# Optimization experiments

Measured on AMD Instinct MI355X. Metric: run time of the kernel, lower is better.

Reference implementation:

```python
import jax, jax.numpy as jnp
import numpy as np

WINDOW = 128  # window_length (overlap-and-add hop); K = 2*WINDOW


def setup_inputs() -> dict:
    key = jax.random.key(0)
    k_x, k_w1, k_b1, k_w2, k_b2 = jax.random.split(key, 5)
    B, D, K, S = 4, 128, 256, 256      # batch, in_channels, segment len, n segments
    C, E, O = 2, 128, 256              # source_num, encoded_frame_dim, out_channels
    x = jax.random.normal(k_x, (B, D, K, S), dtype=jnp.float32)
    prelu_w = jnp.asarray(0.25, dtype=jnp.float32)  # nn.PReLU default init
    conv1_w = jax.random.normal(k_w1, (C * E, D), dtype=jnp.float32) * 0.02
    conv1_b = jax.random.normal(k_b1, (C * E,), dtype=jnp.float32) * 0.02
    conv2_w = jax.random.normal(k_w2, (O, E), dtype=jnp.float32) * 0.02
    conv2_b = jax.random.normal(k_b2, (O,), dtype=jnp.float32) * 0.02
    return {
        "x": x,
        "prelu_w": prelu_w,
        "conv1_w": conv1_w,
        "conv1_b": conv1_b,
        "conv2_w": conv2_w,
        "conv2_b": conv2_b,
        "pad_front": 64,
        "pad_back": 64,
    }


def overlap_and_add(y, hop):
    # y: [B, C, E, S, K] -> [B, C, E, hop*(S-1)+K] windowed scatter-sum
    B, C, E, S, K = y.shape
    T = hop * (S - 1) + K
    idx = (hop * jnp.arange(S)[:, None] + jnp.arange(K)[None, :]).reshape(-1)  # [S*K]
    out = jnp.zeros((B, C, E, T), dtype=y.dtype)
    return out.at[..., idx].add(y.reshape(B, C, E, S * K))


def reference(x, prelu_w, conv1_w, conv1_b, conv2_w, conv2_b, pad_front, pad_back):
    B, D, K, S = x.shape
    E = conv2_w.shape[1]
    C = conv1_w.shape[0] // E
    # PReLU (single shared parameter)
    x = jnp.where(x >= 0, x, prelu_w * x)
    # 1x1 Conv2d: D -> C*E channels (pure GEMM over channel dim)
    x = jnp.einsum('bdks,od->boks', x, conv1_w) + conv1_b[None, :, None, None]
    # split sources/features, move K to last: [B, C, E, S, K]
    x = x.reshape(B, C, E, K, S).transpose(0, 1, 2, 4, 3)
    x = overlap_and_add(x, WINDOW)  # [B, C, E, T]
    T = x.shape[-1]
    end = T - pad_back if pad_back else T  # replicate [pad_front:-pad_back] slicing
    x = x[:, :, :, pad_front:end]          # [B, C, E, L]
    x = jax.nn.relu(x)
    # 1x1 Conv1d: E -> O
    x = jnp.einsum('bcel,oe->bcol', x, conv2_w) + conv2_b[None, None, :, None]
    return x  # [B, C, O, L]
```

## Files before the change

kernel.cpp:

```cpp
#include <hip/hip_runtime.h>
#include <hip/hip_bf16.h>
#include <stdint.h>

#define B_   4
#define D_   128
#define K_   256
#define S_   256
#define O_   256
#define E_   128
#define LOUT 32768

typedef __attribute__((ext_vector_type(8))) short short8;
typedef __attribute__((ext_vector_type(4))) float float4v;

__device__ __forceinline__ unsigned short f2bf(float f) {
  union { float f; unsigned u; } v; v.f = f;
  unsigned r = v.u + 0x7FFF + ((v.u >> 16) & 1);
  return (unsigned short)(r >> 16);
}

__device__ __forceinline__ void gl_lds16(const void* g, void* l) {
  __builtin_amdgcn_global_load_lds(
      (const __attribute__((address_space(1))) void*)g,
      (__attribute__((address_space(3))) void*)l, 16, 0, 0);
}

__global__ void pack_w_kernel(const float* __restrict__ w1, const float* __restrict__ w2,
                              unsigned short* __restrict__ w1p, unsigned short* __restrict__ w2p) {
  int i = blockIdx.x * 256 + threadIdx.x;
  w1p[i] = f2bf(w1[i]);
  w2p[i] = f2bf(w2[i]);
}

__global__ __launch_bounds__(256) void pack_x_kernel(const float* __restrict__ x,
                                                     const float* __restrict__ prelu_w,
                                                     unsigned short* __restrict__ xp) {
  __shared__ float tile[64][65];
  int k  = blockIdx.x;
  int st = blockIdx.y & 3;
  int dt = blockIdx.y >> 2;
  int b  = blockIdx.z;
  float pw = *prelu_w;
  int t = threadIdx.x;

  {
    int sl = t & 63, dl0 = t >> 6;
    const float* src = x + ((size_t)(b * D_) * K_ + k) * S_ + st * 64 + sl;
    for (int i = 0; i < 16; ++i) {
      int dl = dl0 + i * 4;
      float v = src[(size_t)(dt * 64 + dl) * (K_ * S_)];
      tile[dl][sl] = (v >= 0.f) ? v : v * pw;
    }
  }
  __syncthreads();
  {
    int dp = (t & 31) * 2, sl0 = t >> 5;
    for (int i = 0; i < 8; ++i) {
      int sl = sl0 + i * 8;
      int s = st * 64 + sl;
      int d = dt * 64 + dp;
      unsigned v0 = f2bf(tile[dp][sl]);
      unsigned v1 = f2bf(tile[dp + 1][sl]);
      *(unsigned*)(xp + (((size_t)(b * S_ + s) * K_ + k) * D_ + d)) = v0 | (v1 << 16);
    }
  }
}

__global__ __launch_bounds__(256, 2) void fused_kernel(
    const unsigned short* __restrict__ xp,
    const unsigned short* __restrict__ w1p,
    const unsigned short* __restrict__ w2p,
    const float* __restrict__ b1,
    const float* __restrict__ b2,
    float* __restrict__ out) {
  __shared__ __align__(16) unsigned char lds[65536];

  int j = blockIdx.x;
  int b = blockIdx.y;
  int t = threadIdx.x;
  int w  = t >> 6;
  int ln64 = t & 63;
  int q  = ln64 >> 4;
  int ln = ln64 & 15;

  bool va = (j < S_);
  bool vb = (j >= 1);

  {
    bool myv = (w < 2) ? va : vb;
    if (myv) {
      int s = (w < 2) ? j : (j - 1);
      for (int i = 0; i < 16; ++i) {
        int row = (w * 16 + i) * 4 + q;
        int dblk = ln ^ (row & 15);
        const unsigned short* g = xp + (((size_t)(b * S_ + s) * K_ + row) * D_ + dblk * 8);
        gl_lds16((const void*)g, (void*)(lds + (w * 16 + i) * 1024));
      }
    }
  }

  int mtg = w * 4;
  short8 a1[4][4];
  float4v b1v[4];
  for (int m = 0; m < 4; ++m) {
    int o = (mtg + m) * 16 + ln;
    for (int ks = 0; ks < 4; ++ks)
      a1[m][ks] = *(const short8*)(w1p + (size_t)o * D_ + ks * 32 + q * 8);
    b1v[m] = *(const float4v*)(b1 + (mtg + m) * 16 + q * 4);
  }
  float bmul = (va ? 1.f : 0.f) + (vb ? 1.f : 0.f);

  __syncthreads();

  int c = w >> 1;
  int ebase = (w & 1) * 64;

  for (int p = 0; p < 8; ++p) {
    float4v acca[4], accb[4];
    for (int m = 0; m < 4; ++m) { acca[m] = (float4v)0.f; accb[m] = (float4v)0.f; }
    if (va) {
      int row = p * 16 + ln;
      for (int ks = 0; ks < 4; ++ks) {
        short8 bf = *(const short8*)(lds + row * 256 + (((ks * 4 + q) ^ ln) * 16));
        for (int m = 0; m < 4; ++m)
          acca[m] = __builtin_amdgcn_mfma_f32_16x16x32_bf16(a1[m][ks], bf, acca[m], 0, 0, 0);
      }
    }
    if (vb) {
      int row = 128 + p * 16 + ln;
      for (int ks = 0; ks < 4; ++ks) {
        short8 bf = *(const short8*)(lds + row * 256 + (((ks * 4 + q) ^ ln) * 16));
        for (int m = 0; m < 4; ++m)
          accb[m] = __builtin_amdgcn_mfma_f32_16x16x32_bf16(a1[m][ks], bf, accb[m], 0, 0, 0);
      }
    }
    __syncthreads();
    int k1 = p * 16 + ln;
    for (int m = 0; m < 4; ++m) {
      float4v zf = acca[m] + accb[m] + b1v[m] * bmul;
      unsigned long long pk =
          (unsigned long long)f2bf(fmaxf(zf[0], 0.f))
        | ((unsigned long long)f2bf(fmaxf(zf[1], 0.f)) << 16)
        | ((unsigned long long)f2bf(fmaxf(zf[2], 0.f)) << 32)
        | ((unsigned long long)f2bf(fmaxf(zf[3], 0.f)) << 48);
      int e0 = ebase + m * 16 + q * 4;
      *(unsigned long long*)(lds + (c * 128 + k1) * 256 + ((e0 >> 3) ^ ln) * 16 + (e0 & 7) * 2) = pk;
    }
  }
  __syncthreads();

  short8 a2[4][4];
  float4v b2v[4];
  for (int m = 0; m < 4; ++m) {
    int o2 = (mtg + m) * 16 + ln;
    for (int ks = 0; ks < 4; ++ks)
      a2[m][ks] = *(const short8*)(w2p + (size_t)o2 * E_ + ks * 32 + q * 8);
    b2v[m] = *(const float4v*)(b2 + (mtg + m) * 16 + q * 4);
  }

  for (int cc = 0; cc < 2; ++cc) {
    for (int nt = 0; nt < 8; ++nt) {
      float4v acc[4];
      for (int m = 0; m < 4; ++m) acc[m] = (float4v)0.f;
      int k1 = nt * 16 + ln;
      for (int ks = 0; ks < 4; ++ks) {
        short8 bf = *(const short8*)(lds + (cc * 128 + k1) * 256 + (((ks * 4 + q) ^ ln) * 16));
        for (int m = 0; m < 4; ++m)
          acc[m] = __builtin_amdgcn_mfma_f32_16x16x32_bf16(a2[m][ks], bf, acc[m], 0, 0, 0);
      }
      int lpos = j * 128 + k1 - 64;
      if (lpos >= 0 && lpos < LOUT) {
        for (int m = 0; m < 4; ++m) {
          float4v ov = acc[m] + b2v[m];
          for (int r = 0; r < 4; ++r) {
            int o2 = (mtg + m) * 16 + q * 4 + r;
            out[((size_t)(b * 2 + cc) * 256 + o2) * LOUT + lpos] = ov[r];
          }
        }
      }
    }
  }
}

extern "C" void kernel_launch(void* const* d_in, const int* in_sizes, int n_in,
                              void* d_out, int out_size, void* d_ws, size_t ws_size,
                              hipStream_t stream) {
  const float* x       = (const float*)d_in[0];
  const float* prelu_w = (const float*)d_in[1];
  const float* w1      = (const float*)d_in[2];
  const float* b1      = (const float*)d_in[3];
  const float* w2      = (const float*)d_in[4];
  const float* b2      = (const float*)d_in[5];

  unsigned short* xp  = (unsigned short*)d_ws;
  unsigned short* w1p = xp + (size_t)B_ * S_ * K_ * D_;
  unsigned short* w2p = w1p + (size_t)O_ * D_;

  pack_w_kernel<<<dim3(128), 256, 0, stream>>>(w1, w2, w1p, w2p);
  pack_x_kernel<<<dim3(K_, 8, B_), 256, 0, stream>>>(x, prelu_w, xp);
  fused_kernel<<<dim3(S_ + 1, B_), 256, 0, stream>>>(xp, w1p, w2p, b1, b2,
                                                     (float*)d_out);
}
```

Measured before the change: 437.1 us.

## Vectorize pack loads/stores and swap GEMM2 operands for float4 output stores

```diff
diff --git a/kernel.cpp b/kernel.cpp
--- a/kernel.cpp
+++ b/kernel.cpp
@@ -44,24 +44,32 @@
   int t = threadIdx.x;
 
   {
-    int sl = t & 63, dl0 = t >> 6;
-    const float* src = x + ((size_t)(b * D_) * K_ + k) * S_ + st * 64 + sl;
-    for (int i = 0; i < 16; ++i) {
-      int dl = dl0 + i * 4;
-      float v = src[(size_t)(dt * 64 + dl) * (K_ * S_)];
-      tile[dl][sl] = (v >= 0.f) ? v : v * pw;
+    int s4  = (t & 15) * 4;
+    int dl0 = t >> 4;
+    const float* src = x + ((size_t)(b * D_ + dt * 64) * K_ + k) * S_ + st * 64 + s4;
+#pragma unroll
+    for (int i = 0; i < 4; ++i) {
+      int dl = dl0 + i * 16;
+      float4v v = *(const float4v*)(src + (size_t)dl * (K_ * S_));
+#pragma unroll
+      for (int r = 0; r < 4; ++r) {
+        float f = v[r];
+        tile[dl][s4 + r] = (f >= 0.f) ? f : f * pw;
+      }
     }
   }
   __syncthreads();
   {
-    int dp = (t & 31) * 2, sl0 = t >> 5;
-    for (int i = 0; i < 8; ++i) {
-      int sl = sl0 + i * 8;
+    int d8 = (t & 7) * 8;
+    int sx = t >> 3;
+#pragma unroll
+    for (int i = 0; i < 2; ++i) {
+      int sl = sx + i * 32;
+      short8 o;
+#pragma unroll
+      for (int e = 0; e < 8; ++e) o[e] = (short)f2bf(tile[d8 + e][sl]);
       int s = st * 64 + sl;
-      int d = dt * 64 + dp;
-      unsigned v0 = f2bf(tile[dp][sl]);
-      unsigned v1 = f2bf(tile[dp + 1][sl]);
-      *(unsigned*)(xp + (((size_t)(b * S_ + s) * K_ + k) * D_ + d)) = v0 | (v1 << 16);
+      *(short8*)(xp + (((size_t)(b * S_ + s) * K_ + k) * D_ + dt * 64 + d8)) = o;
     }
   }
 }
@@ -147,35 +155,40 @@
       *(unsigned long long*)(lds + (c * 128 + k1) * 256 + ((e0 >> 3) ^ ln) * 16 + (e0 & 7) * 2) = pk;
     }
   }
+
+  short8 w2f[4][4];
+  float  b2s[4];
+  for (int n = 0; n < 4; ++n) {
+    int o2 = w * 64 + n * 16 + ln;
+    for (int ks = 0; ks < 4; ++ks)
+      w2f[n][ks] = *(const short8*)(w2p + (size_t)o2 * E_ + ks * 32 + q * 8);
+    b2s[n] = b2[o2];
+  }
+
   __syncthreads();
 
-  short8 a2[4][4];
-  float4v b2v[4];
-  for (int m = 0; m < 4; ++m) {
-    int o2 = (mtg + m) * 16 + ln;
-    for (int ks = 0; ks < 4; ++ks)
-      a2[m][ks] = *(const short8*)(w2p + (size_t)o2 * E_ + ks * 32 + q * 8);
-    b2v[m] = *(const float4v*)(b2 + (mtg + m) * 16 + q * 4);
-  }
-
   for (int cc = 0; cc < 2; ++cc) {
-    for (int nt = 0; nt < 8; ++nt) {
+    for (int m = 0; m < 8; ++m) {
+      short8 zf[4];
+#pragma unroll
+      for (int ks = 0; ks < 4; ++ks)
+        zf[ks] = *(const short8*)(lds + (cc * 128 + m * 16 + ln) * 256 + (((ks * 4 + q) ^ ln) * 16));
       float4v acc[4];
-      for (int m = 0; m < 4; ++m) acc[m] = (float4v)0.f;
-      int k1 = nt * 16 + ln;
-      for (int ks = 0; ks < 4; ++ks) {
-        short8 bf = *(const short8*)(lds + (cc * 128 + k1) * 256 + (((ks * 4 + q) ^ ln) * 16));
-        for (int m = 0; m < 4; ++m)
-          acc[m] = __builtin_amdgcn_mfma_f32_16x16x32_bf16(a2[m][ks], bf, acc[m], 0, 0, 0);
-      }
-      int lpos = j * 128 + k1 - 64;
+#pragma unroll
+      for (int n = 0; n < 4; ++n) acc[n] = (float4v)0.f;
+#pragma unroll
+      for (int ks = 0; ks < 4; ++ks)
+#pragma unroll
+        for (int n = 0; n < 4; ++n)
+          acc[n] = __builtin_amdgcn_mfma_f32_16x16x32_bf16(zf[ks], w2f[n][ks], acc[n], 0, 0, 0);
+      int lpos = j * 128 + m * 16 + q * 4 - 64;
       if (lpos >= 0 && lpos < LOUT) {
-        for (int m = 0; m < 4; ++m) {
-          float4v ov = acc[m] + b2v[m];
-          for (int r = 0; r < 4; ++r) {
-            int o2 = (mtg + m) * 16 + q * 4 + r;
-            out[((size_t)(b * 2 + cc) * 256 + o2) * LOUT + lpos] = ov[r];
-          }
+#pragma unroll
+        for (int n = 0; n < 4; ++n) {
+          float4v sv;
+#pragma unroll
+          for (int r = 0; r < 4; ++r) sv[r] = acc[n][r] + b2s[n];
+          *(float4v*)(out + ((size_t)(b * 2 + cc) * 256 + w * 64 + n * 16 + ln) * LOUT + lpos) = sv;
         }
       }
     }
```

After: 426.7 us. 1.02x faster.
